# Optimization experiments

Measured on AMD Instinct MI355X. Metric: run time of the kernel, lower is better.

## Reference

```python
import jax, jax.numpy as jnp
import numpy as np

B, F, NQ, DT, TS, K = 16384, 256, 2048, 256, 16, 8
GH, SH, CALH = 128, 128, 16
SPD = DT + TS
SPH = max(int(SPD * 0.25), 16)
CD = DT + 3 + TS + 3  # h_base + y_base + 3 gate stats + z_top + |d_safe| + |d_spec| = 278
CH = max(int(CD * 0.25), 16)
RES_SCALE = 0.1


def _ln(x, g, b):
    m = x.mean(-1, keepdims=True)
    v = ((x - m) ** 2).mean(-1, keepdims=True)
    return (x - m) * jax.lax.rsqrt(v + 1e-5) * g + b


def _resmlp(x, lg, lb, w1, b1, w2, b2):
    h = jnp.maximum(_ln(x, lg, lb) @ w1 + b1, 0.0)
    return h @ w2 + b2


def setup_inputs() -> dict:
    key = jax.random.key(0)
    ks = iter(jax.random.split(key, 48))
    def nrm(shape, s=0.05):
        return jax.random.normal(next(ks), shape, jnp.float32) * s
    d = {}
    d["x_num"] = jax.random.normal(next(ks), (B, F), jnp.float32)
    d["robust_center"] = nrm((1, F), 0.1)
    d["robust_scale"] = jax.random.uniform(next(ks), (1, F), jnp.float32, 0.5, 1.5)
    d["quantile_sorted"] = jnp.sort(jax.random.normal(next(ks), (NQ, F), jnp.float32), axis=0)
    d["stem_w1"] = nrm((3, CALH)); d["stem_b1"] = jnp.zeros((CALH,))
    d["stem_w2"] = nrm((CALH, CALH)); d["stem_b2"] = jnp.zeros((CALH,))
    d["stem_w3"] = nrm((CALH, 1)); d["stem_b3"] = jnp.zeros((1,))
    d["gate_w1"] = nrm((F, GH)); d["gate_b1"] = jnp.zeros((GH,))
    d["gate_w2"] = nrm((GH, F)); d["gate_b2"] = jnp.zeros((F,))
    d["bb_w"] = nrm((F, DT)); d["bb_b"] = jnp.zeros((DT,))
    d["base_w"] = nrm((DT, 1)); d["base_b"] = jnp.zeros((1,))
    d["safe_lg"] = jnp.ones((DT,)); d["safe_lb"] = jnp.zeros((DT,))
    d["safe_w1"] = nrm((DT, SH)); d["safe_b1"] = jnp.zeros((SH,))
    d["safe_w2"] = nrm((SH, 1)); d["safe_b2"] = jnp.zeros((1,))
    d["top_w1"] = nrm((1, TS)); d["top_b1"] = jnp.zeros((TS,))
    d["top_w2"] = nrm((TS, TS)); d["top_b2"] = jnp.zeros((TS,))
    d["spec_lg"] = jnp.ones((SPD,)); d["spec_lb"] = jnp.zeros((SPD,))
    d["spec_w1"] = nrm((SPD, SPH)); d["spec_b1"] = jnp.zeros((SPH,))
    d["spec_w2"] = nrm((SPH, 1)); d["spec_b2"] = jnp.zeros((1,))
    d["conf_lg"] = jnp.ones((CD,)); d["conf_lb"] = jnp.zeros((CD,))
    d["conf_w1"] = nrm((CD, CH)); d["conf_b1"] = jnp.zeros((CH,))
    d["conf_w2"] = nrm((CH, 1)); d["conf_b2"] = jnp.full((1,), -2.0)  # gamma_init_bias
    return d


def _forward(x_num, robust_center, robust_scale, quantile_sorted,
             stem_w1, stem_b1, stem_w2, stem_b2, stem_w3, stem_b3,
             gate_w1, gate_b1, gate_w2, gate_b2,
             bb_w, bb_b, base_w, base_b,
             safe_lg, safe_lb, safe_w1, safe_b1, safe_w2, safe_b2,
             top_w1, top_b1, top_w2, top_b2,
             spec_lg, spec_lb, spec_w1, spec_b1, spec_w2, spec_b2,
             conf_lg, conf_lb, conf_w1, conf_b1, conf_w2, conf_b2):
    # --- calibration views ---
    x_robust = (x_num - robust_center) / robust_scale
    ranks = jax.vmap(jnp.searchsorted, in_axes=(1, 1), out_axes=1)(
        jax.lax.stop_gradient(quantile_sorted), jax.lax.stop_gradient(x_num))  # [B,F] int
    x_quant = jnp.clip(ranks.astype(jnp.float32) / (NQ - 1.0), 0.0, 1.0)
    x_views = jnp.stack([x_num, x_robust, x_quant], axis=-1)  # [B,F,3]
    h = jnp.maximum(x_views @ stem_w1 + stem_b1, 0.0)
    h = jnp.maximum(h @ stem_w2 + stem_b2, 0.0)
    resid = jnp.tanh((h @ stem_w3 + stem_b3)[..., 0])
    x_cal = x_num + RES_SCALE * resid
    # --- input gate ---
    g = jax.nn.sigmoid(jnp.maximum(x_cal @ gate_w1 + gate_b1, 0.0) @ gate_w2 + gate_b2)
    x_gated = x_cal * g
    # --- backbone (stand-in for TMLPBackbone.encode_hidden) ---
    h_base = jnp.maximum(x_gated @ bb_w + bb_b, 0.0)  # [B,DT]
    y_base = h_base @ base_w + base_b  # [B,1]
    gate_mean = g.mean(axis=1, keepdims=True)
    gate_max = g.max(axis=1, keepdims=True)
    gate_std = g.std(axis=1, keepdims=True)  # ddof=0, matches unbiased=False
    delta_safe = _resmlp(h_base, safe_lg, safe_lb, safe_w1, safe_b1, safe_w2, safe_b2)
    # --- top-k feature gather ---
    topk_g, topk_idx = jax.lax.top_k(g, K)
    topk_x = jnp.take_along_axis(x_cal, topk_idx, axis=1)
    topk_w = topk_g / (topk_g.sum(axis=1, keepdims=True) + 1e-6)
    xw = (topk_x * topk_w)[..., None]  # [B,K,1]
    tok = jnp.maximum(xw @ top_w1 + top_b1, 0.0) @ top_w2 + top_b2  # [B,K,TS]
    z_top = tok.mean(axis=1)  # [B,TS]
    delta_spec = _resmlp(jnp.concatenate([h_base, z_top], axis=1),
                         spec_lg, spec_lb, spec_w1, spec_b1, spec_w2, spec_b2)
    conf_in = jnp.concatenate([h_base, y_base, gate_mean, gate_max, gate_std,
                               z_top, jnp.abs(delta_safe), jnp.abs(delta_spec)], axis=1)
    gamma = jax.nn.sigmoid(_resmlp(conf_in, conf_lg, conf_lb, conf_w1, conf_b1, conf_w2, conf_b2))
    return (y_base + delta_safe + gamma * delta_spec)[:, 0]


def reference(x_num, robust_center, robust_scale, quantile_sorted,
              stem_w1, stem_b1, stem_w2, stem_b2, stem_w3, stem_b3,
              gate_w1, gate_b1, gate_w2, gate_b2,
              bb_w, bb_b, base_w, base_b,
              safe_lg, safe_lb, safe_w1, safe_b1, safe_w2, safe_b2,
              top_w1, top_b1, top_w2, top_b2,
              spec_lg, spec_lb, spec_w1, spec_b1, spec_w2, spec_b2,
              conf_lg, conf_lb, conf_w1, conf_b1, conf_w2, conf_b2):
    return _forward(x_num, robust_center, robust_scale, quantile_sorted,
                    stem_w1, stem_b1, stem_w2, stem_b2, stem_w3, stem_b3,
                    gate_w1, gate_b1, gate_w2, gate_b2,
                    bb_w, bb_b, base_w, base_b,
                    safe_lg, safe_lb, safe_w1, safe_b1, safe_w2, safe_b2,
                    top_w1, top_b1, top_w2, top_b2,
                    spec_lg, spec_lb, spec_w1, spec_b1, spec_w2, spec_b2,
                    conf_lg, conf_lb, conf_w1, conf_b1, conf_w2, conf_b2)
```

## Files before the change

kernel.cpp:

```cpp
#include <hip/hip_runtime.h>
#include <math.h>

static constexpr int B  = 16384;
static constexpr int F  = 256;
static constexpr int NQ = 2048;
static constexpr int TS = 16;
static constexpr int KTOP = 8;
static constexpr int SPD = 272;
static constexpr int SPH = 68;
static constexpr int CD  = 278;
static constexpr int CH  = 69;

typedef __attribute__((ext_vector_type(8))) short bf16x8;
typedef __attribute__((ext_vector_type(4))) float f32x4;

__device__ inline short f2bf(float f) {
    unsigned u = __builtin_bit_cast(unsigned, f);
    unsigned r = (u + 0x7FFF + ((u >> 16) & 1)) >> 16;
    return (short)r;
}
__device__ inline float bf2f(short s) {
    return __builtin_bit_cast(float, ((unsigned)(unsigned short)s) << 16);
}

__device__ inline float fast_tanh(float o) {
    o = fminf(fmaxf(o, -15.0f), 15.0f);
    float e = __expf(2.0f * o);
    return (e - 1.0f) / (e + 1.0f);
}

__device__ inline void prep_one(const float* W, short* T, int local,
                                int K, int N, int KP) {
    const int n = local / KP, k = local - n * KP;
    T[local] = (k < K && n < N) ? f2bf(W[k * N + n]) : (short)0;
}

__global__ __launch_bounds__(256) void k_prepall(
    const float* __restrict__ gate_w1, const float* __restrict__ gate_w2,
    const float* __restrict__ bb_w,    const float* __restrict__ safe_w1,
    const float* __restrict__ spec_w1, const float* __restrict__ conf_w1,
    const float* __restrict__ qs,
    short* __restrict__ w1t, short* __restrict__ w2t, short* __restrict__ bbt,
    short* __restrict__ sw1t, short* __restrict__ spw1t, short* __restrict__ cfw1t,
    float* __restrict__ qs_t)
{
    const int idx = blockIdx.x * 256 + threadIdx.x;
    if (idx < 32768)       prep_one(gate_w1, w1t,  idx,           256, 128, 256);
    else if (idx < 65536)  prep_one(gate_w2, w2t,  idx - 32768,   128, 256, 128);
    else if (idx < 131072) prep_one(bb_w,    bbt,  idx - 65536,   256, 256, 256);
    else if (idx < 163840) prep_one(safe_w1, sw1t, idx - 131072,  256, 128, 256);
    else if (idx < 200704) prep_one(spec_w1, spw1t, idx - 163840, 272, 68, 288);
    else if (idx < 237568) prep_one(conf_w1, cfw1t, idx - 200704, 278, 69, 288);
    else if (idx < 761856) {
        const int local = idx - 237568;
        const int f = local >> 11, q = local & 2047;
        qs_t[local] = qs[q * 256 + f];
    }
}

__global__ __launch_bounds__(256) void k_calib9(
    const float* __restrict__ x_num, const float* __restrict__ center,
    const float* __restrict__ scale, const float* __restrict__ qs,
    const float* __restrict__ qs_t,
    const float* __restrict__ sw1, const float* __restrict__ sb1,
    const float* __restrict__ sw2, const float* __restrict__ sb2,
    const float* __restrict__ sw3, const float* __restrict__ sb3,
    short* __restrict__ x_bf)
{
    __shared__ float cq[63 * 128];
    const int tid = threadIdx.x;
    const int fl = tid & 127;
    const int half = tid >> 7;
    const int fg = blockIdx.y;
    const int f = fg * 128 + fl;

    for (int idx = tid; idx < 63 * 128; idx += 256) {
        const int j = idx >> 7, f2 = idx & 127;
        cq[idx] = qs[(32 * (j + 1)) * 256 + fg * 128 + f2];
    }
    __syncthreads();

    const float c = center[f];
    const float inv_sc = 1.0f / scale[f];
    const float* colp = qs_t + (long)f * NQ;
    const long row_base = (long)blockIdx.x * 32 + half * 16;

#pragma unroll 1
    for (int grp = 0; grp < 2; ++grp) {
        const long r0 = row_base + grp * 8;
        float x[8], xr[8];
#pragma unroll
        for (int i = 0; i < 8; ++i) {
            x[i] = x_num[(r0 + i) * F + f];
            xr[i] = (x[i] - c) * inv_sc;
        }
        int lo[8], hi[8];
#pragma unroll
        for (int i = 0; i < 8; ++i) { lo[i] = 0; hi[i] = 63; }
#pragma unroll
        for (int it = 0; it < 6; ++it) {
            float qv[8]; int mid[8];
#pragma unroll
            for (int i = 0; i < 8; ++i) {
                mid[i] = (lo[i] + hi[i]) >> 1;
                qv[i] = cq[mid[i] * 128 + fl];
            }
#pragma unroll
            for (int i = 0; i < 8; ++i) {
                if (qv[i] < x[i]) lo[i] = mid[i] + 1; else hi[i] = mid[i];
            }
        }
        int base[8];
        {
            float pm[8];
#pragma unroll
            for (int i = 0; i < 8; ++i) pm[i] = colp[lo[i] * 32 + 16];
#pragma unroll
            for (int i = 0; i < 8; ++i)
                base[i] = lo[i] * 32 + ((pm[i] < x[i]) ? 16 : 0);
        }
        float xq[8];
#pragma unroll
        for (int i = 0; i < 8; ++i) {
            const float4* wp = reinterpret_cast<const float4*>(&colp[base[i]]);
            const float4 a = wp[0], b = wp[1], d = wp[2], e = wp[3];
            int cN = 0;
            cN += (a.x < x[i]); cN += (a.y < x[i]); cN += (a.z < x[i]); cN += (a.w < x[i]);
            cN += (b.x < x[i]); cN += (b.y < x[i]); cN += (b.z < x[i]); cN += (b.w < x[i]);
            cN += (d.x < x[i]); cN += (d.y < x[i]); cN += (d.z < x[i]); cN += (d.w < x[i]);
            cN += (e.x < x[i]); cN += (e.y < x[i]); cN += (e.z < x[i]); cN += (e.w < x[i]);
            const int rank = base[i] + cN;
            xq[i] = fminf((float)rank * (1.0f / (float)(NQ - 1)), 1.0f);
        }
#pragma unroll
        for (int hgrp = 0; hgrp < 2; ++hgrp) {
            const int o4 = hgrp * 4;
            float h2[4][16];
#pragma unroll
            for (int j = 0; j < 16; ++j) {
                const float bb = sb2[j];
#pragma unroll
                for (int i = 0; i < 4; ++i) h2[i][j] = bb;
            }
#pragma unroll 4
            for (int i16 = 0; i16 < 16; ++i16) {
                const float w0 = sw1[i16], w1v = sw1[16 + i16], w2v = sw1[32 + i16];
                const float bb = sb1[i16];
                float h1v[4];
#pragma unroll
                for (int i = 0; i < 4; ++i)
                    h1v[i] = fmaxf(bb + x[o4 + i] * w0 + xr[o4 + i] * w1v + xq[o4 + i] * w2v, 0.0f);
                float wv[16];
                const float4* wr = reinterpret_cast<const float4*>(&sw2[i16 * 16]);
                *reinterpret_cast<float4*>(&wv[0])  = wr[0];
                *reinterpret_cast<float4*>(&wv[4])  = wr[1];
                *reinterpret_cast<float4*>(&wv[8])  = wr[2];
                *reinterpret_cast<float4*>(&wv[12]) = wr[3];
#pragma unroll
                for (int j = 0; j < 16; ++j) {
#pragma unroll
                    for (int i = 0; i < 4; ++i) h2[i][j] += h1v[i] * wv[j];
                }
            }
            const float b3 = sb3[0];
            float o[4] = {b3, b3, b3, b3};
#pragma unroll
            for (int j = 0; j < 16; ++j) {
                const float w3v = sw3[j];
#pragma unroll
                for (int i = 0; i < 4; ++i) o[i] += fmaxf(h2[i][j], 0.0f) * w3v;
            }
#pragma unroll
            for (int i = 0; i < 4; ++i) {
                const float xc = x[o4 + i] + 0.1f * fast_tanh(o[i]);
                x_bf[(r0 + o4 + i) * F + f] = f2bf(xc);
            }
        }
    }
}

static constexpr int ST1 = 136;
static constexpr int ST2 = 264;

__global__ __launch_bounds__(256) void k_fused(
    const short* __restrict__ x_bf,
    const short* __restrict__ w1t, const float* __restrict__ gate_b1,
    const short* __restrict__ w2t, const float* __restrict__ gate_b2,
    const short* __restrict__ bbt, const float* __restrict__ bb_b,
    float* __restrict__ g, float* __restrict__ h_b)
{
    __shared__ short s_c1[32 * ST1];
    __shared__ short s_xg[32 * ST2];

    const int tid = threadIdx.x;
    const int wave = tid >> 6, lane = tid & 63;
    const int sub = lane & 15, quad = lane >> 4;
    const int wm = wave & 1, wn = wave >> 1;
    const long row0 = (long)blockIdx.x * 32;
    const long mrow = row0 + wm * 16 + sub;

    {
        f32x4 acc[4];
#pragma unroll
        for (int t = 0; t < 4; ++t) acc[t] = (f32x4){0, 0, 0, 0};
#pragma unroll
        for (int k0 = 0; k0 < 256; k0 += 32) {
            const bf16x8 af = *reinterpret_cast<const bf16x8*>(
                &x_bf[mrow * 256 + k0 + quad * 8]);
#pragma unroll
            for (int t = 0; t < 4; ++t) {
                const int col = wn * 64 + t * 16 + sub;
                const bf16x8 bf = *reinterpret_cast<const bf16x8*>(
                    &w1t[(long)col * 256 + k0 + quad * 8]);
                acc[t] = __builtin_amdgcn_mfma_f32_16x16x32_bf16(af, bf, acc[t], 0, 0, 0);
            }
        }
#pragma unroll
        for (int t = 0; t < 4; ++t) {
            const int col = wn * 64 + t * 16 + sub;
            const float bb = gate_b1[col];
#pragma unroll
            for (int r = 0; r < 4; ++r) {
                const int rowl = wm * 16 + quad * 4 + r;
                s_c1[rowl * ST1 + col] = f2bf(fmaxf(acc[t][r] + bb, 0.0f));
            }
        }
    }
    __syncthreads();

    {
        f32x4 acc[8];
#pragma unroll
        for (int t = 0; t < 8; ++t) acc[t] = (f32x4){0, 0, 0, 0};
#pragma unroll
        for (int k0 = 0; k0 < 128; k0 += 32) {
            const bf16x8 af = *reinterpret_cast<const bf16x8*>(
                &s_c1[(wm * 16 + sub) * ST1 + k0 + quad * 8]);
#pragma unroll
            for (int t = 0; t < 8; ++t) {
                const int col = wn * 128 + t * 16 + sub;
                const bf16x8 bf = *reinterpret_cast<const bf16x8*>(
                    &w2t[(long)col * 128 + k0 + quad * 8]);
                acc[t] = __builtin_amdgcn_mfma_f32_16x16x32_bf16(af, bf, acc[t], 0, 0, 0);
            }
        }
#pragma unroll
        for (int t = 0; t < 8; ++t) {
            const int col = wn * 128 + t * 16 + sub;
            const float bb = gate_b2[col];
#pragma unroll
            for (int r = 0; r < 4; ++r) {
                const int rowl = wm * 16 + quad * 4 + r;
                const float gv = 1.0f / (1.0f + __expf(-(acc[t][r] + bb)));
                g[(row0 + rowl) * 256 + col] = gv;
                const float xv = bf2f(x_bf[(row0 + rowl) * 256 + col]);
                s_xg[rowl * ST2 + col] = f2bf(xv * gv);
            }
        }
    }
    __syncthreads();

    {
        f32x4 acc[8];
#pragma unroll
        for (int t = 0; t < 8; ++t) acc[t] = (f32x4){0, 0, 0, 0};
#pragma unroll
        for (int k0 = 0; k0 < 256; k0 += 32) {
            const bf16x8 af = *reinterpret_cast<const bf16x8*>(
                &s_xg[(wm * 16 + sub) * ST2 + k0 + quad * 8]);
#pragma unroll
            for (int t = 0; t < 8; ++t) {
                const int col = wn * 128 + t * 16 + sub;
                const bf16x8 bf = *reinterpret_cast<const bf16x8*>(
                    &bbt[(long)col * 256 + k0 + quad * 8]);
                acc[t] = __builtin_amdgcn_mfma_f32_16x16x32_bf16(af, bf, acc[t], 0, 0, 0);
            }
        }
#pragma unroll
        for (int t = 0; t < 8; ++t) {
            const int col = wn * 128 + t * 16 + sub;
            const float bb = bb_b[col];
#pragma unroll
            for (int r = 0; r < 4; ++r) {
                const int rowl = wm * 16 + quad * 4 + r;
                h_b[(row0 + rowl) * 256 + col] = fmaxf(acc[t][r] + bb, 0.0f);
            }
        }
    }
}

__global__ __launch_bounds__(256) void k_topk2(
    const float* __restrict__ g, const short* __restrict__ x_bf,
    const float* __restrict__ tw1, const float* __restrict__ tb1,
    const float* __restrict__ tw2, const float* __restrict__ tb2,
    float* __restrict__ z_top, float* __restrict__ stats)
{
    const int wave = threadIdx.x >> 6, lane = threadIdx.x & 63;
    const long b = (long)blockIdx.x * 4 + wave;
    const long base = b * F;

    float gv[4];
#pragma unroll
    for (int i = 0; i < 4; ++i) gv[i] = g[base + lane + 64 * i];

    float s = gv[0] + gv[1] + gv[2] + gv[3];
    float mx = fmaxf(fmaxf(gv[0], gv[1]), fmaxf(gv[2], gv[3]));
    for (int m = 32; m; m >>= 1) {
        s  += __shfl_xor(s, m);
        mx  = fmaxf(mx, __shfl_xor(mx, m));
    }
    const float mean = s * (1.0f / 256.0f);
    float vs = 0.0f;
#pragma unroll
    for (int i = 0; i < 4; ++i) { float d = gv[i] - mean; vs += d * d; }
    for (int m = 32; m; m >>= 1) vs += __shfl_xor(vs, m);
    const float stdv = sqrtf(vs * (1.0f / 256.0f));

    float cur[4]; int curi[4];
#pragma unroll
    for (int i = 0; i < 4; ++i) { cur[i] = gv[i]; curi[i] = lane + 64 * i; }
    float tv[KTOP]; int ti[KTOP]; float vsum = 0.0f;
    for (int r = 0; r < KTOP; ++r) {
        float bv = cur[0]; int bi = curi[0];
#pragma unroll
        for (int i = 1; i < 4; ++i)
            if (cur[i] > bv || (cur[i] == bv && curi[i] < bi)) { bv = cur[i]; bi = curi[i]; }
        for (int m = 32; m; m >>= 1) {
            float ov = __shfl_xor(bv, m);
            int   oi = __shfl_xor(bi, m);
            if (ov > bv || (ov == bv && oi < bi)) { bv = ov; bi = oi; }
        }
        tv[r] = bv; ti[r] = bi; vsum += bv;
#pragma unroll
        for (int i = 0; i < 4; ++i) if (curi[i] == bi) cur[i] = -INFINITY;
    }
    const float denom = 1.0f / (vsum + 1e-6f);

    float hm = 0.0f;
    if (lane < 16) {
        for (int k = 0; k < KTOP; ++k) {
            const float xk = bf2f(x_bf[base + ti[k]]);
            const float xw = xk * (tv[k] * denom);
            hm += fmaxf(xw * tw1[lane] + tb1[lane], 0.0f);
        }
        hm *= (1.0f / (float)KTOP);
    }
    float z = (lane < 16) ? tb2[lane] : 0.0f;
#pragma unroll
    for (int j = 0; j < 16; ++j) {
        const float hj = __shfl(hm, j);
        if (lane < 16) z += hj * tw2[j * 16 + lane];
    }
    if (lane < 16) z_top[b * TS + lane] = z;
    if (lane == 0) {
        stats[b * 4 + 0] = mean;
        stats[b * 4 + 1] = mx;
        stats[b * 4 + 2] = stdv;
    }
}

static constexpr int HST = 260;
static constexpr int AST = 312;

template<int KP>
__device__ __forceinline__ void head_mfma16(
    const short* sa, const short* __restrict__ Wt,
    const float* __restrict__ b1v, const float* __restrict__ w2v, int Nreal,
    float (*s_red)[16], int wave, int sub, int quad)
{
    f32x4 acc[2];
#pragma unroll
    for (int t = 0; t < 2; ++t) acc[t] = (f32x4){0, 0, 0, 0};
#pragma unroll
    for (int k0 = 0; k0 < KP; k0 += 32) {
        const bf16x8 af = *reinterpret_cast<const bf16x8*>(
            &sa[sub * AST + k0 + quad * 8]);
#pragma unroll
        for (int t = 0; t < 2; ++t) {
            const int col = wave * 32 + t * 16 + sub;
            const bf16x8 bf = *reinterpret_cast<const bf16x8*>(
                &Wt[(long)col * KP + k0 + quad * 8]);
            acc[t] = __builtin_amdgcn_mfma_f32_16x16x32_bf16(af, bf, acc[t], 0, 0, 0);
        }
    }
    float rsum[4] = {0, 0, 0, 0};
#pragma unroll
    for (int t = 0; t < 2; ++t) {
        const int col = wave * 32 + t * 16 + sub;
        const float bb = (col < Nreal) ? b1v[col] : 0.0f;
        const float ww = (col < Nreal) ? w2v[col] : 0.0f;
#pragma unroll
        for (int rr = 0; rr < 4; ++rr)
            rsum[rr] += fmaxf(acc[t][rr] + bb, 0.0f) * ww;
    }
#pragma unroll
    for (int rr = 0; rr < 4; ++rr)
        for (int m = 1; m < 16; m <<= 1) rsum[rr] += __shfl_xor(rsum[rr], m);
    if (sub == 0) {
#pragma unroll
        for (int rr = 0; rr < 4; ++rr)
            s_red[wave][quad * 4 + rr] = rsum[rr];
    }
}

__global__ __launch_bounds__(256) void k_tail3(
    const float* __restrict__ h_base, const float* __restrict__ z_top,
    const float* __restrict__ gstats,
    const float* __restrict__ base_w, const float* __restrict__ base_b,
    const float* __restrict__ safe_lg, const float* __restrict__ safe_lb,
    const short* __restrict__ sw1t, const float* __restrict__ safe_b1,
    const float* __restrict__ safe_w2, const float* __restrict__ safe_b2,
    const float* __restrict__ spec_lg, const float* __restrict__ spec_lb,
    const short* __restrict__ spw1t, const float* __restrict__ spec_b1,
    const float* __restrict__ spec_w2, const float* __restrict__ spec_b2,
    const float* __restrict__ conf_lg, const float* __restrict__ conf_lb,
    const short* __restrict__ cfw1t, const float* __restrict__ conf_b1,
    const float* __restrict__ conf_w2, const float* __restrict__ conf_b2,
    float* __restrict__ out)
{
    __shared__ float s_h[16 * HST];
    __shared__ short s_a[16 * AST];
    __shared__ float s_z[16 * 16];
    __shared__ float s_g[16 * 4];
    __shared__ float s_sc[16 * 14];
    __shared__ float s_red[4][16];

    const int tid = threadIdx.x;
    const int wave = tid >> 6, lane = tid & 63;
    const int sub = lane & 15, quad = lane >> 4;
    const long row0 = (long)blockIdx.x * 16;

    for (int idx = tid; idx < 16 * 64; idx += 256) {
        const int r = idx >> 6, q = idx & 63;
        *reinterpret_cast<float4*>(&s_h[r * HST + q * 4]) =
            *reinterpret_cast<const float4*>(&h_base[(row0 + r) * 256 + q * 4]);
    }
    if (tid < 256) s_z[tid] = z_top[row0 * 16 + tid];
    if (tid < 64) s_g[tid] = gstats[row0 * 4 + tid];
    __syncthreads();

    {
        const int r = tid >> 4, l16 = tid & 15;
        float S = 0.0f, SS = 0.0f, Y = 0.0f;
#pragma unroll
        for (int i = 0; i < 16; ++i) {
            const int k = l16 + 16 * i;
            const float v = s_h[r * HST + k];
            S += v; SS += v * v; Y += v * base_w[k];
        }
        const float z0 = s_z[r * 16 + l16];
        float Sz = z0, SSz = z0 * z0;
#pragma unroll
        for (int m = 1; m < 16; m <<= 1) {
            S += __shfl_xor(S, m); SS += __shfl_xor(SS, m); Y += __shfl_xor(Y, m);
            Sz += __shfl_xor(Sz, m); SSz += __shfl_xor(SSz, m);
        }
        if (l16 == 0) {
            float* sc = &s_sc[r * 14];
            sc[0] = S; sc[1] = SS; sc[2] = Sz; sc[3] = SSz;
            sc[4] = Y + base_b[0];
            const float mu = S * (1.0f / 256.0f);
            sc[5] = mu;
            sc[6] = rsqrtf(SS * (1.0f / 256.0f) - mu * mu + 1e-5f);
            const float musp = (S + Sz) * (1.0f / (float)SPD);
            sc[7] = musp;
            sc[8] = rsqrtf((SS + SSz) * (1.0f / (float)SPD) - musp * musp + 1e-5f);
        }
    }
    __syncthreads();

    for (int idx = tid; idx < 16 * 128; idx += 256) {
        const int r = idx >> 7, k = (idx & 127) * 2;
        const float mu = s_sc[r * 14 + 5], rs = s_sc[r * 14 + 6];
        const float v0 = (s_h[r * HST + k] - mu) * rs * safe_lg[k] + safe_lb[k];
        const float v1 = (s_h[r * HST + k + 1] - mu) * rs * safe_lg[k + 1] + safe_lb[k + 1];
        const unsigned pk = (unsigned)(unsigned short)f2bf(v0) |
                            ((unsigned)(unsigned short)f2bf(v1) << 16);
        *reinterpret_cast<unsigned*>(&s_a[r * AST + k]) = pk;
    }
    __syncthreads();

    head_mfma16<256>(s_a, sw1t, safe_b1, safe_w2, 128, s_red, wave, sub, quad);
    __syncthreads();

    if (tid < 16)
        s_sc[tid * 14 + 9] = s_red[0][tid] + s_red[1][tid] + s_red[2][tid] + s_red[3][tid] + safe_b2[0];
    for (int idx = tid; idx < 16 * 144; idx += 256) {
        const int r = idx / 144, k = (idx - r * 144) * 2;
        const float mu = s_sc[r * 14 + 7], rs = s_sc[r * 14 + 8];
        float vv[2];
#pragma unroll
        for (int h = 0; h < 2; ++h) {
            const int kk = k + h;
            float raw = (kk < 256) ? s_h[r * HST + kk]
                       : (kk < SPD) ? s_z[r * 16 + kk - 256] : 0.0f;
            vv[h] = (kk < SPD) ? (raw - mu) * rs * spec_lg[kk] + spec_lb[kk] : 0.0f;
        }
        const unsigned pk = (unsigned)(unsigned short)f2bf(vv[0]) |
                            ((unsigned)(unsigned short)f2bf(vv[1]) << 16);
        *reinterpret_cast<unsigned*>(&s_a[r * AST + k]) = pk;
    }
    __syncthreads();

    head_mfma16<288>(s_a, spw1t, spec_b1, spec_w2, SPH, s_red, wave, sub, quad);
    __syncthreads();

    if (tid < 16) {
        float* sc = &s_sc[tid * 14];
        const float dsp = s_red[0][tid] + s_red[1][tid] + s_red[2][tid] + s_red[3][tid] + spec_b2[0];
        sc[10] = dsp;
        const float yb = sc[4];
        const float gm = s_g[tid * 4 + 0], gx = s_g[tid * 4 + 1], gs = s_g[tid * 4 + 2];
        const float ads = fabsf(sc[9]), adp = fabsf(dsp);
        const float es = yb + gm + gx + gs + ads + adp;
        const float eq = yb * yb + gm * gm + gx * gx + gs * gs + ads * ads + adp * adp;
        const float muc = (sc[0] + sc[2] + es) * (1.0f / (float)CD);
        sc[11] = muc;
        sc[12] = rsqrtf((sc[1] + sc[3] + eq) * (1.0f / (float)CD) - muc * muc + 1e-5f);
    }
    __syncthreads();

    for (int idx = tid; idx < 16 * 144; idx += 256) {
        const int r = idx / 144, k = (idx - r * 144) * 2;
        const float mu = s_sc[r * 14 + 11], rs = s_sc[r * 14 + 12];
        float vv[2];
#pragma unroll
        for (int h = 0; h < 2; ++h) {
            const int kk = k + h;
            float raw;
            if (kk < 256)       raw = s_h[r * HST + kk];
            else if (kk == 256) raw = s_sc[r * 14 + 4];
            else if (kk == 257) raw = s_g[r * 4 + 0];
            else if (kk == 258) raw = s_g[r * 4 + 1];
            else if (kk == 259) raw = s_g[r * 4 + 2];
            else if (kk < 276)  raw = s_z[r * 16 + kk - 260];
            else if (kk == 276) raw = fabsf(s_sc[r * 14 + 9]);
            else if (kk == 277) raw = fabsf(s_sc[r * 14 + 10]);
            else                raw = 0.0f;
            vv[h] = (kk < CD) ? (raw - mu) * rs * conf_lg[kk] + conf_lb[kk] : 0.0f;
        }
        const unsigned pk = (unsigned)(unsigned short)f2bf(vv[0]) |
                            ((unsigned)(unsigned short)f2bf(vv[1]) << 16);
        *reinterpret_cast<unsigned*>(&s_a[r * AST + k]) = pk;
    }
    __syncthreads();

    head_mfma16<288>(s_a, cfw1t, conf_b1, conf_w2, CH, s_red, wave, sub, quad);
    __syncthreads();

    if (tid < 16) {
        const float* sc = &s_sc[tid * 14];
        const float gamma = 1.0f / (1.0f + __expf(
            -(s_red[0][tid] + s_red[1][tid] + s_red[2][tid] + s_red[3][tid] + conf_b2[0])));
        out[row0 + tid] = sc[4] + sc[9] + gamma * sc[10];
    }
}

extern "C" void kernel_launch(void* const* d_in, const int* in_sizes, int n_in,
                              void* d_out, int out_size, void* d_ws, size_t ws_size,
                              hipStream_t stream)
{
    const float* x_num   = (const float*)d_in[0];
    const float* center  = (const float*)d_in[1];
    const float* scale   = (const float*)d_in[2];
    const float* qs      = (const float*)d_in[3];
    const float* stem_w1 = (const float*)d_in[4];
    const float* stem_b1 = (const float*)d_in[5];
    const float* stem_w2 = (const float*)d_in[6];
    const float* stem_b2 = (const float*)d_in[7];
    const float* stem_w3 = (const float*)d_in[8];
    const float* stem_b3 = (const float*)d_in[9];
    const float* gate_w1 = (const float*)d_in[10];
    const float* gate_b1 = (const float*)d_in[11];
    const float* gate_w2 = (const float*)d_in[12];
    const float* gate_b2 = (const float*)d_in[13];
    const float* bb_w    = (const float*)d_in[14];
    const float* bb_b    = (const float*)d_in[15];
    const float* base_w  = (const float*)d_in[16];
    const float* base_b  = (const float*)d_in[17];
    const float* safe_lg = (const float*)d_in[18];
    const float* safe_lb = (const float*)d_in[19];
    const float* safe_w1 = (const float*)d_in[20];
    const float* safe_b1 = (const float*)d_in[21];
    const float* safe_w2 = (const float*)d_in[22];
    const float* safe_b2 = (const float*)d_in[23];
    const float* top_w1  = (const float*)d_in[24];
    const float* top_b1  = (const float*)d_in[25];
    const float* top_w2  = (const float*)d_in[26];
    const float* top_b2  = (const float*)d_in[27];
    const float* spec_lg = (const float*)d_in[28];
    const float* spec_lb = (const float*)d_in[29];
    const float* spec_w1 = (const float*)d_in[30];
    const float* spec_b1 = (const float*)d_in[31];
    const float* spec_w2 = (const float*)d_in[32];
    const float* spec_b2 = (const float*)d_in[33];
    const float* conf_lg = (const float*)d_in[34];
    const float* conf_lb = (const float*)d_in[35];
    const float* conf_w1 = (const float*)d_in[36];
    const float* conf_b1 = (const float*)d_in[37];
    const float* conf_w2 = (const float*)d_in[38];
    const float* conf_b2 = (const float*)d_in[39];

    float* ws    = (float*)d_ws;
    float* x_cal = ws;
    float* g_h   = x_cal + (long)B * 256;
    float* g     = g_h   + (long)B * 128;
    float* h_b   = g     + (long)B * 256;
    float* z_top = h_b   + (long)B * 256;
    float* gstat = z_top + (long)B * 16;
    short* w1t   = (short*)(gstat + (long)B * 4);
    short* w2t   = w1t   + 128 * 256;
    short* bbt   = w2t   + 256 * 128;
    short* sw1t  = bbt   + 256 * 256;
    short* spw1t = sw1t  + 128 * 256;
    short* cfw1t = spw1t + 128 * 288;
    float* qs_t  = h_b;
    short* x_bf  = (short*)g_h;
    float* out   = (float*)d_out;

    k_prepall<<<2976, 256, 0, stream>>>(gate_w1, gate_w2, bb_w, safe_w1, spec_w1,
                                        conf_w1, qs,
                                        w1t, w2t, bbt, sw1t, spw1t, cfw1t, qs_t);
    k_calib9<<<dim3(512, 2), 256, 0, stream>>>(x_num, center, scale, qs, qs_t,
                                               stem_w1, stem_b1, stem_w2, stem_b2,
                                               stem_w3, stem_b3, x_bf);
    k_fused<<<512, 256, 0, stream>>>(x_bf, w1t, gate_b1, w2t, gate_b2, bbt, bb_b,
                                     g, h_b);
    k_topk2<<<B / 4, 256, 0, stream>>>(g, x_bf, top_w1, top_b1, top_w2, top_b2,
                                       z_top, gstat);
    k_tail3<<<B / 16, 256, 0, stream>>>(h_b, z_top, gstat,
                                        base_w, base_b,
                                        safe_lg, safe_lb, sw1t, safe_b1, safe_w2, safe_b2,
                                        spec_lg, spec_lb, spw1t, spec_b1, spec_w2, spec_b2,
                                        conf_lg, conf_lb, cfw1t, conf_b1, conf_w2, conf_b2,
                                        out);
}
```

Before: 314.1 us.

## Fuse gate MLP, top-k, backbone and heads into one kernel

Merges the gate/backbone GEMM kernel, the per-row top-k kernel and the tail heads kernel into one kernel processing 16 rows per block. The gate values and backbone activations stay in shared memory (backbone stored as bf16) instead of round-tripping g and h_b through global memory. Row statistics are reduced directly from the MFMA epilogue. This removes two launches and large intermediate global traffic, but halves the rows per block for the GEMMs, so weight reuse per block drops. It also adds bf16 rounding of h_base before the layer norms.

```diff
diff --git a/kernel.cpp b/kernel.cpp
--- a/kernel.cpp
+++ b/kernel.cpp
@@ -179,188 +179,11 @@
     }
 }
 
-static constexpr int ST1 = 136;
-static constexpr int ST2 = 264;
-
-__global__ __launch_bounds__(256) void k_fused(
-    const short* __restrict__ x_bf,
-    const short* __restrict__ w1t, const float* __restrict__ gate_b1,
-    const short* __restrict__ w2t, const float* __restrict__ gate_b2,
-    const short* __restrict__ bbt, const float* __restrict__ bb_b,
-    float* __restrict__ g, float* __restrict__ h_b)
-{
-    __shared__ short s_c1[32 * ST1];
-    __shared__ short s_xg[32 * ST2];
-
-    const int tid = threadIdx.x;
-    const int wave = tid >> 6, lane = tid & 63;
-    const int sub = lane & 15, quad = lane >> 4;
-    const int wm = wave & 1, wn = wave >> 1;
-    const long row0 = (long)blockIdx.x * 32;
-    const long mrow = row0 + wm * 16 + sub;
-
-    {
-        f32x4 acc[4];
-#pragma unroll
-        for (int t = 0; t < 4; ++t) acc[t] = (f32x4){0, 0, 0, 0};
-#pragma unroll
-        for (int k0 = 0; k0 < 256; k0 += 32) {
-            const bf16x8 af = *reinterpret_cast<const bf16x8*>(
-                &x_bf[mrow * 256 + k0 + quad * 8]);
-#pragma unroll
-            for (int t = 0; t < 4; ++t) {
-                const int col = wn * 64 + t * 16 + sub;
-                const bf16x8 bf = *reinterpret_cast<const bf16x8*>(
-                    &w1t[(long)col * 256 + k0 + quad * 8]);
-                acc[t] = __builtin_amdgcn_mfma_f32_16x16x32_bf16(af, bf, acc[t], 0, 0, 0);
-            }
-        }
-#pragma unroll
-        for (int t = 0; t < 4; ++t) {
-            const int col = wn * 64 + t * 16 + sub;
-            const float bb = gate_b1[col];
-#pragma unroll
-            for (int r = 0; r < 4; ++r) {
-                const int rowl = wm * 16 + quad * 4 + r;
-                s_c1[rowl * ST1 + col] = f2bf(fmaxf(acc[t][r] + bb, 0.0f));
-            }
-        }
-    }
-    __syncthreads();
-
-    {
-        f32x4 acc[8];
-#pragma unroll
-        for (int t = 0; t < 8; ++t) acc[t] = (f32x4){0, 0, 0, 0};
-#pragma unroll
-        for (int k0 = 0; k0 < 128; k0 += 32) {
-            const bf16x8 af = *reinterpret_cast<const bf16x8*>(
-                &s_c1[(wm * 16 + sub) * ST1 + k0 + quad * 8]);
-#pragma unroll
-            for (int t = 0; t < 8; ++t) {
-                const int col = wn * 128 + t * 16 + sub;
-                const bf16x8 bf = *reinterpret_cast<const bf16x8*>(
-                    &w2t[(long)col * 128 + k0 + quad * 8]);
-                acc[t] = __builtin_amdgcn_mfma_f32_16x16x32_bf16(af, bf, acc[t], 0, 0, 0);
-            }
-        }
-#pragma unroll
-        for (int t = 0; t < 8; ++t) {
-            const int col = wn * 128 + t * 16 + sub;
-            const float bb = gate_b2[col];
-#pragma unroll
-            for (int r = 0; r < 4; ++r) {
-                const int rowl = wm * 16 + quad * 4 + r;
-                const float gv = 1.0f / (1.0f + __expf(-(acc[t][r] + bb)));
-                g[(row0 + rowl) * 256 + col] = gv;
-                const float xv = bf2f(x_bf[(row0 + rowl) * 256 + col]);
-                s_xg[rowl * ST2 + col] = f2bf(xv * gv);
-            }
-        }
-    }
-    __syncthreads();
-
-    {
-        f32x4 acc[8];
-#pragma unroll
-        for (int t = 0; t < 8; ++t) acc[t] = (f32x4){0, 0, 0, 0};
-#pragma unroll
-        for (int k0 = 0; k0 < 256; k0 += 32) {
-            const bf16x8 af = *reinterpret_cast<const bf16x8*>(
-                &s_xg[(wm * 16 + sub) * ST2 + k0 + quad * 8]);
-#pragma unroll
-            for (int t = 0; t < 8; ++t) {
-                const int col = wn * 128 + t * 16 + sub;
-                const bf16x8 bf = *reinterpret_cast<const bf16x8*>(
-                    &bbt[(long)col * 256 + k0 + quad * 8]);
-                acc[t] = __builtin_amdgcn_mfma_f32_16x16x32_bf16(af, bf, acc[t], 0, 0, 0);
-            }
-        }
-#pragma unroll
-        for (int t = 0; t < 8; ++t) {
-            const int col = wn * 128 + t * 16 + sub;
-            const float bb = bb_b[col];
-#pragma unroll
-            for (int r = 0; r < 4; ++r) {
-                const int rowl = wm * 16 + quad * 4 + r;
-                h_b[(row0 + rowl) * 256 + col] = fmaxf(acc[t][r] + bb, 0.0f);
-            }
-        }
-    }
-}
-
-__global__ __launch_bounds__(256) void k_topk2(
-    const float* __restrict__ g, const short* __restrict__ x_bf,
-    const float* __restrict__ tw1, const float* __restrict__ tb1,
-    const float* __restrict__ tw2, const float* __restrict__ tb2,
-    float* __restrict__ z_top, float* __restrict__ stats)
-{
-    const int wave = threadIdx.x >> 6, lane = threadIdx.x & 63;
-    const long b = (long)blockIdx.x * 4 + wave;
-    const long base = b * F;
-
-    float gv[4];
-#pragma unroll
-    for (int i = 0; i < 4; ++i) gv[i] = g[base + lane + 64 * i];
-
-    float s = gv[0] + gv[1] + gv[2] + gv[3];
-    float mx = fmaxf(fmaxf(gv[0], gv[1]), fmaxf(gv[2], gv[3]));
-    for (int m = 32; m; m >>= 1) {
-        s  += __shfl_xor(s, m);
-        mx  = fmaxf(mx, __shfl_xor(mx, m));
-    }
-    const float mean = s * (1.0f / 256.0f);
-    float vs = 0.0f;
-#pragma unroll
-    for (int i = 0; i < 4; ++i) { float d = gv[i] - mean; vs += d * d; }
-    for (int m = 32; m; m >>= 1) vs += __shfl_xor(vs, m);
-    const float stdv = sqrtf(vs * (1.0f / 256.0f));
-
-    float cur[4]; int curi[4];
-#pragma unroll
-    for (int i = 0; i < 4; ++i) { cur[i] = gv[i]; curi[i] = lane + 64 * i; }
-    float tv[KTOP]; int ti[KTOP]; float vsum = 0.0f;
-    for (int r = 0; r < KTOP; ++r) {
-        float bv = cur[0]; int bi = curi[0];
-#pragma unroll
-        for (int i = 1; i < 4; ++i)
-            if (cur[i] > bv || (cur[i] == bv && curi[i] < bi)) { bv = cur[i]; bi = curi[i]; }
-        for (int m = 32; m; m >>= 1) {
-            float ov = __shfl_xor(bv, m);
-            int   oi = __shfl_xor(bi, m);
-            if (ov > bv || (ov == bv && oi < bi)) { bv = ov; bi = oi; }
-        }
-        tv[r] = bv; ti[r] = bi; vsum += bv;
-#pragma unroll
-        for (int i = 0; i < 4; ++i) if (curi[i] == bi) cur[i] = -INFINITY;
-    }
-    const float denom = 1.0f / (vsum + 1e-6f);
-
-    float hm = 0.0f;
-    if (lane < 16) {
-        for (int k = 0; k < KTOP; ++k) {
-            const float xk = bf2f(x_bf[base + ti[k]]);
-            const float xw = xk * (tv[k] * denom);
-            hm += fmaxf(xw * tw1[lane] + tb1[lane], 0.0f);
-        }
-        hm *= (1.0f / (float)KTOP);
-    }
-    float z = (lane < 16) ? tb2[lane] : 0.0f;
-#pragma unroll
-    for (int j = 0; j < 16; ++j) {
-        const float hj = __shfl(hm, j);
-        if (lane < 16) z += hj * tw2[j * 16 + lane];
-    }
-    if (lane < 16) z_top[b * TS + lane] = z;
-    if (lane == 0) {
-        stats[b * 4 + 0] = mean;
-        stats[b * 4 + 1] = mx;
-        stats[b * 4 + 2] = stdv;
-    }
-}
-
-static constexpr int HST = 260;
-static constexpr int AST = 312;
+static constexpr int MR   = 16;
+static constexpr int GST  = 260;
+static constexpr int AST  = 312;
+static constexpr int HBST = 264;
+static constexpr int C1ST = 136;
 
 template<int KP>
 __device__ __forceinline__ void head_mfma16(
@@ -403,10 +226,14 @@
     }
 }
 
-__global__ __launch_bounds__(256) void k_tail3(
-    const float* __restrict__ h_base, const float* __restrict__ z_top,
-    const float* __restrict__ gstats,
+__global__ __launch_bounds__(256) void k_mega(
+    const short* __restrict__ x_bf,
+    const short* __restrict__ w1t, const float* __restrict__ gate_b1,
+    const short* __restrict__ w2t, const float* __restrict__ gate_b2,
+    const short* __restrict__ bbt, const float* __restrict__ bb_b,
     const float* __restrict__ base_w, const float* __restrict__ base_b,
+    const float* __restrict__ tw1, const float* __restrict__ tb1,
+    const float* __restrict__ tw2, const float* __restrict__ tb2,
     const float* __restrict__ safe_lg, const float* __restrict__ safe_lb,
     const short* __restrict__ sw1t, const float* __restrict__ safe_b1,
     const float* __restrict__ safe_w2, const float* __restrict__ safe_b2,
@@ -418,99 +245,269 @@
     const float* __restrict__ conf_w2, const float* __restrict__ conf_b2,
     float* __restrict__ out)
 {
-    __shared__ float s_h[16 * HST];
-    __shared__ short s_a[16 * AST];
-    __shared__ float s_z[16 * 16];
-    __shared__ float s_g[16 * 4];
-    __shared__ float s_sc[16 * 14];
-    __shared__ float s_red[4][16];
+    __shared__ float s_g[MR * GST];
+    __shared__ short s_u1[MR * AST];
+    __shared__ short s_c1[MR * C1ST];
+    __shared__ short s_hbb[MR * HBST];
+    __shared__ float s_z[MR * 16];
+    __shared__ float s_sc[MR * 16];
+    __shared__ float s_redS[4][16], s_redSS[4][16], s_redY[4][16];
 
     const int tid = threadIdx.x;
     const int wave = tid >> 6, lane = tid & 63;
     const int sub = lane & 15, quad = lane >> 4;
-    const long row0 = (long)blockIdx.x * 16;
-
-    for (int idx = tid; idx < 16 * 64; idx += 256) {
-        const int r = idx >> 6, q = idx & 63;
-        *reinterpret_cast<float4*>(&s_h[r * HST + q * 4]) =
-            *reinterpret_cast<const float4*>(&h_base[(row0 + r) * 256 + q * 4]);
-    }
-    if (tid < 256) s_z[tid] = z_top[row0 * 16 + tid];
-    if (tid < 64) s_g[tid] = gstats[row0 * 4 + tid];
-    __syncthreads();
+    const long row0 = (long)blockIdx.x * MR;
 
     {
-        const int r = tid >> 4, l16 = tid & 15;
-        float S = 0.0f, SS = 0.0f, Y = 0.0f;
-#pragma unroll
-        for (int i = 0; i < 16; ++i) {
-            const int k = l16 + 16 * i;
-            const float v = s_h[r * HST + k];
-            S += v; SS += v * v; Y += v * base_w[k];
-        }
-        const float z0 = s_z[r * 16 + l16];
-        float Sz = z0, SSz = z0 * z0;
+        f32x4 acc[2];
+#pragma unroll
+        for (int t = 0; t < 2; ++t) acc[t] = (f32x4){0, 0, 0, 0};
+#pragma unroll
+        for (int k0 = 0; k0 < 256; k0 += 32) {
+            const bf16x8 af = *reinterpret_cast<const bf16x8*>(
+                &x_bf[(row0 + sub) * 256 + k0 + quad * 8]);
+#pragma unroll
+            for (int t = 0; t < 2; ++t) {
+                const int col = wave * 32 + t * 16 + sub;
+                const bf16x8 bf = *reinterpret_cast<const bf16x8*>(
+                    &w1t[(long)col * 256 + k0 + quad * 8]);
+                acc[t] = __builtin_amdgcn_mfma_f32_16x16x32_bf16(af, bf, acc[t], 0, 0, 0);
+            }
+        }
+#pragma unroll
+        for (int t = 0; t < 2; ++t) {
+            const int col = wave * 32 + t * 16 + sub;
+            const float bb = gate_b1[col];
+#pragma unroll
+            for (int r = 0; r < 4; ++r)
+                s_c1[(quad * 4 + r) * C1ST + col] = f2bf(fmaxf(acc[t][r] + bb, 0.0f));
+        }
+    }
+    __syncthreads();
+
+    {
+        f32x4 acc[4];
+#pragma unroll
+        for (int t = 0; t < 4; ++t) acc[t] = (f32x4){0, 0, 0, 0};
+#pragma unroll
+        for (int k0 = 0; k0 < 128; k0 += 32) {
+            const bf16x8 af = *reinterpret_cast<const bf16x8*>(
+                &s_c1[sub * C1ST + k0 + quad * 8]);
+#pragma unroll
+            for (int t = 0; t < 4; ++t) {
+                const int col = wave * 64 + t * 16 + sub;
+                const bf16x8 bf = *reinterpret_cast<const bf16x8*>(
+                    &w2t[(long)col * 128 + k0 + quad * 8]);
+                acc[t] = __builtin_amdgcn_mfma_f32_16x16x32_bf16(af, bf, acc[t], 0, 0, 0);
+            }
+        }
+#pragma unroll
+        for (int t = 0; t < 4; ++t) {
+            const int col = wave * 64 + t * 16 + sub;
+            const float bb = gate_b2[col];
+#pragma unroll
+            for (int r = 0; r < 4; ++r)
+                s_g[(quad * 4 + r) * GST + col] =
+                    1.0f / (1.0f + __expf(-(acc[t][r] + bb)));
+        }
+    }
+    __syncthreads();
+
+#pragma unroll 1
+    for (int rr = 0; rr < 4; ++rr) {
+        const int row = wave * 4 + rr;
+        float gv[4];
+#pragma unroll
+        for (int i = 0; i < 4; ++i) gv[i] = s_g[row * GST + lane + 64 * i];
+
+        float s = gv[0] + gv[1] + gv[2] + gv[3];
+        float mx = fmaxf(fmaxf(gv[0], gv[1]), fmaxf(gv[2], gv[3]));
+        for (int m = 32; m; m >>= 1) {
+            s  += __shfl_xor(s, m);
+            mx  = fmaxf(mx, __shfl_xor(mx, m));
+        }
+        const float mean = s * (1.0f / 256.0f);
+        float vs = 0.0f;
+#pragma unroll
+        for (int i = 0; i < 4; ++i) { float d = gv[i] - mean; vs += d * d; }
+        for (int m = 32; m; m >>= 1) vs += __shfl_xor(vs, m);
+        const float stdv = sqrtf(vs * (1.0f / 256.0f));
+
+        float cur[4]; int curi[4];
+#pragma unroll
+        for (int i = 0; i < 4; ++i) { cur[i] = gv[i]; curi[i] = lane + 64 * i; }
+        float tv[KTOP]; int ti[KTOP]; float vsum = 0.0f;
+        for (int r = 0; r < KTOP; ++r) {
+            float bv = cur[0]; int bi = curi[0];
+#pragma unroll
+            for (int i = 1; i < 4; ++i)
+                if (cur[i] > bv || (cur[i] == bv && curi[i] < bi)) { bv = cur[i]; bi = curi[i]; }
+            for (int m = 32; m; m >>= 1) {
+                float ov = __shfl_xor(bv, m);
+                int   oi = __shfl_xor(bi, m);
+                if (ov > bv || (ov == bv && oi < bi)) { bv = ov; bi = oi; }
+            }
+            tv[r] = bv; ti[r] = bi; vsum += bv;
+#pragma unroll
+            for (int i = 0; i < 4; ++i) if (curi[i] == bi) cur[i] = -INFINITY;
+        }
+        const float denom = 1.0f / (vsum + 1e-6f);
+
+        float hm = 0.0f;
+        if (lane < 16) {
+            for (int k = 0; k < KTOP; ++k) {
+                const float xk = bf2f(x_bf[(row0 + row) * 256 + ti[k]]);
+                const float xw = xk * (tv[k] * denom);
+                hm += fmaxf(xw * tw1[lane] + tb1[lane], 0.0f);
+            }
+            hm *= (1.0f / (float)KTOP);
+        }
+        float z = (lane < 16) ? tb2[lane] : 0.0f;
+#pragma unroll
+        for (int j = 0; j < 16; ++j) {
+            const float hj = __shfl(hm, j);
+            if (lane < 16) z += hj * tw2[j * 16 + lane];
+        }
+        if (lane < 16) s_z[row * 16 + lane] = z;
+        float zz = (lane < 16) ? z : 0.0f;
+        float zz2 = zz * zz;
 #pragma unroll
         for (int m = 1; m < 16; m <<= 1) {
-            S += __shfl_xor(S, m); SS += __shfl_xor(SS, m); Y += __shfl_xor(Y, m);
-            Sz += __shfl_xor(Sz, m); SSz += __shfl_xor(SSz, m);
-        }
-        if (l16 == 0) {
-            float* sc = &s_sc[r * 14];
-            sc[0] = S; sc[1] = SS; sc[2] = Sz; sc[3] = SSz;
-            sc[4] = Y + base_b[0];
-            const float mu = S * (1.0f / 256.0f);
-            sc[5] = mu;
-            sc[6] = rsqrtf(SS * (1.0f / 256.0f) - mu * mu + 1e-5f);
-            const float musp = (S + Sz) * (1.0f / (float)SPD);
-            sc[7] = musp;
-            sc[8] = rsqrtf((SS + SSz) * (1.0f / (float)SPD) - musp * musp + 1e-5f);
-        }
-    }
-    __syncthreads();
-
-    for (int idx = tid; idx < 16 * 128; idx += 256) {
+            zz += __shfl_xor(zz, m); zz2 += __shfl_xor(zz2, m);
+        }
+        if (lane == 0) {
+            float* sc = &s_sc[row * 16];
+            sc[2] = zz; sc[3] = zz2;
+            sc[13] = mean; sc[14] = mx; sc[15] = stdv;
+        }
+    }
+    __syncthreads();
+
+    for (int idx = tid; idx < MR * 128; idx += 256) {
         const int r = idx >> 7, k = (idx & 127) * 2;
-        const float mu = s_sc[r * 14 + 5], rs = s_sc[r * 14 + 6];
-        const float v0 = (s_h[r * HST + k] - mu) * rs * safe_lg[k] + safe_lb[k];
-        const float v1 = (s_h[r * HST + k + 1] - mu) * rs * safe_lg[k + 1] + safe_lb[k + 1];
+        const unsigned xp = *reinterpret_cast<const unsigned*>(
+            &x_bf[(row0 + r) * 256 + k]);
+        const float x0 = bf2f((short)(xp & 0xFFFF));
+        const float x1 = bf2f((short)(xp >> 16));
+        const float v0 = x0 * s_g[r * GST + k];
+        const float v1 = x1 * s_g[r * GST + k + 1];
         const unsigned pk = (unsigned)(unsigned short)f2bf(v0) |
                             ((unsigned)(unsigned short)f2bf(v1) << 16);
-        *reinterpret_cast<unsigned*>(&s_a[r * AST + k]) = pk;
-    }
-    __syncthreads();
-
-    head_mfma16<256>(s_a, sw1t, safe_b1, safe_w2, 128, s_red, wave, sub, quad);
-    __syncthreads();
-
-    if (tid < 16)
-        s_sc[tid * 14 + 9] = s_red[0][tid] + s_red[1][tid] + s_red[2][tid] + s_red[3][tid] + safe_b2[0];
-    for (int idx = tid; idx < 16 * 144; idx += 256) {
+        *reinterpret_cast<unsigned*>(&s_u1[r * AST + k]) = pk;
+    }
+    __syncthreads();
+
+    {
+        f32x4 acc[4];
+#pragma unroll
+        for (int t = 0; t < 4; ++t) acc[t] = (f32x4){0, 0, 0, 0};
+#pragma unroll
+        for (int k0 = 0; k0 < 256; k0 += 32) {
+            const bf16x8 af = *reinterpret_cast<const bf16x8*>(
+                &s_u1[sub * AST + k0 + quad * 8]);
+#pragma unroll
+            for (int t = 0; t < 4; ++t) {
+                const int col = wave * 64 + t * 16 + sub;
+                const bf16x8 bf = *reinterpret_cast<const bf16x8*>(
+                    &bbt[(long)col * 256 + k0 + quad * 8]);
+                acc[t] = __builtin_amdgcn_mfma_f32_16x16x32_bf16(af, bf, acc[t], 0, 0, 0);
+            }
+        }
+        float Sp[4] = {0,0,0,0}, SSp[4] = {0,0,0,0}, Yp[4] = {0,0,0,0};
+#pragma unroll
+        for (int t = 0; t < 4; ++t) {
+            const int col = wave * 64 + t * 16 + sub;
+            const float bb = bb_b[col];
+            const float bw = base_w[col];
+#pragma unroll
+            for (int r = 0; r < 4; ++r) {
+                const float h = fmaxf(acc[t][r] + bb, 0.0f);
+                s_hbb[(quad * 4 + r) * HBST + col] = f2bf(h);
+                Sp[r] += h; SSp[r] += h * h; Yp[r] += h * bw;
+            }
+        }
+#pragma unroll
+        for (int r = 0; r < 4; ++r) {
+#pragma unroll
+            for (int m = 1; m < 16; m <<= 1) {
+                Sp[r] += __shfl_xor(Sp[r], m);
+                SSp[r] += __shfl_xor(SSp[r], m);
+                Yp[r] += __shfl_xor(Yp[r], m);
+            }
+        }
+        if (sub == 0) {
+#pragma unroll
+            for (int r = 0; r < 4; ++r) {
+                s_redS[wave][quad * 4 + r] = Sp[r];
+                s_redSS[wave][quad * 4 + r] = SSp[r];
+                s_redY[wave][quad * 4 + r] = Yp[r];
+            }
+        }
+    }
+    __syncthreads();
+
+    if (tid < MR) {
+        float S = 0, SS = 0, Y = 0;
+#pragma unroll
+        for (int w = 0; w < 4; ++w) {
+            S += s_redS[w][tid]; SS += s_redSS[w][tid]; Y += s_redY[w][tid];
+        }
+        float* sc = &s_sc[tid * 16];
+        sc[0] = S; sc[1] = SS;
+        sc[4] = Y + base_b[0];
+        const float mu = S * (1.0f / 256.0f);
+        sc[5] = mu;
+        sc[6] = rsqrtf(SS * (1.0f / 256.0f) - mu * mu + 1e-5f);
+        const float musp = (S + sc[2]) * (1.0f / (float)SPD);
+        sc[7] = musp;
+        sc[8] = rsqrtf((SS + sc[3]) * (1.0f / (float)SPD) - musp * musp + 1e-5f);
+    }
+    __syncthreads();
+
+    for (int idx = tid; idx < MR * 128; idx += 256) {
+        const int r = idx >> 7, k = (idx & 127) * 2;
+        const float mu = s_sc[r * 16 + 5], rs = s_sc[r * 16 + 6];
+        const float h0 = bf2f(s_hbb[r * HBST + k]);
+        const float h1 = bf2f(s_hbb[r * HBST + k + 1]);
+        const float v0 = (h0 - mu) * rs * safe_lg[k] + safe_lb[k];
+        const float v1 = (h1 - mu) * rs * safe_lg[k + 1] + safe_lb[k + 1];
+        const unsigned pk = (unsigned)(unsigned short)f2bf(v0) |
+                            ((unsigned)(unsigned short)f2bf(v1) << 16);
+        *reinterpret_cast<unsigned*>(&s_u1[r * AST + k]) = pk;
+    }
+    __syncthreads();
+    head_mfma16<256>(s_u1, sw1t, safe_b1, safe_w2, 128, s_redS, wave, sub, quad);
+    __syncthreads();
+
+    if (tid < MR)
+        s_sc[tid * 16 + 9] = s_redS[0][tid] + s_redS[1][tid] + s_redS[2][tid] +
+                             s_redS[3][tid] + safe_b2[0];
+    for (int idx = tid; idx < MR * 144; idx += 256) {
         const int r = idx / 144, k = (idx - r * 144) * 2;
-        const float mu = s_sc[r * 14 + 7], rs = s_sc[r * 14 + 8];
+        const float mu = s_sc[r * 16 + 7], rs = s_sc[r * 16 + 8];
         float vv[2];
 #pragma unroll
         for (int h = 0; h < 2; ++h) {
             const int kk = k + h;
-            float raw = (kk < 256) ? s_h[r * HST + kk]
+            float raw = (kk < 256) ? bf2f(s_hbb[r * HBST + kk])
                        : (kk < SPD) ? s_z[r * 16 + kk - 256] : 0.0f;
             vv[h] = (kk < SPD) ? (raw - mu) * rs * spec_lg[kk] + spec_lb[kk] : 0.0f;
         }
         const unsigned pk = (unsigned)(unsigned short)f2bf(vv[0]) |
                             ((unsigned)(unsigned short)f2bf(vv[1]) << 16);
-        *reinterpret_cast<unsigned*>(&s_a[r * AST + k]) = pk;
-    }
-    __syncthreads();
-
-    head_mfma16<288>(s_a, spw1t, spec_b1, spec_w2, SPH, s_red, wave, sub, quad);
-    __syncthreads();
-
-    if (tid < 16) {
-        float* sc = &s_sc[tid * 14];
-        const float dsp = s_red[0][tid] + s_red[1][tid] + s_red[2][tid] + s_red[3][tid] + spec_b2[0];
+        *reinterpret_cast<unsigned*>(&s_u1[r * AST + k]) = pk;
+    }
+    __syncthreads();
+    head_mfma16<288>(s_u1, spw1t, spec_b1, spec_w2, SPH, s_redS, wave, sub, quad);
+    __syncthreads();
+
+    if (tid < MR) {
+        float* sc = &s_sc[tid * 16];
+        const float dsp = s_redS[0][tid] + s_redS[1][tid] + s_redS[2][tid] +
+                          s_redS[3][tid] + spec_b2[0];
         sc[10] = dsp;
         const float yb = sc[4];
-        const float gm = s_g[tid * 4 + 0], gx = s_g[tid * 4 + 1], gs = s_g[tid * 4 + 2];
+        const float gm = sc[13], gx = sc[14], gs = sc[15];
         const float ads = fabsf(sc[9]), adp = fabsf(dsp);
         const float es = yb + gm + gx + gs + ads + adp;
         const float eq = yb * yb + gm * gm + gx * gx + gs * gs + ads * ads + adp * adp;
@@ -520,38 +517,37 @@
     }
     __syncthreads();
 
-    for (int idx = tid; idx < 16 * 144; idx += 256) {
+    for (int idx = tid; idx < MR * 144; idx += 256) {
         const int r = idx / 144, k = (idx - r * 144) * 2;
-        const float mu = s_sc[r * 14 + 11], rs = s_sc[r * 14 + 12];
+        const float mu = s_sc[r * 16 + 11], rs = s_sc[r * 16 + 12];
         float vv[2];
 #pragma unroll
         for (int h = 0; h < 2; ++h) {
             const int kk = k + h;
             float raw;
-            if (kk < 256)       raw = s_h[r * HST + kk];
-            else if (kk == 256) raw = s_sc[r * 14 + 4];
-            else if (kk == 257) raw = s_g[r * 4 + 0];
-            else if (kk == 258) raw = s_g[r * 4 + 1];
-            else if (kk == 259) raw = s_g[r * 4 + 2];
+            if (kk < 256)       raw = bf2f(s_hbb[r * HBST + kk]);
+            else if (kk == 256) raw = s_sc[r * 16 + 4];
+            else if (kk == 257) raw = s_sc[r * 16 + 13];
+            else if (kk == 258) raw = s_sc[r * 16 + 14];
+            else if (kk == 259) raw = s_sc[r * 16 + 15];
             else if (kk < 276)  raw = s_z[r * 16 + kk - 260];
-            else if (kk == 276) raw = fabsf(s_sc[r * 14 + 9]);
-            else if (kk == 277) raw = fabsf(s_sc[r * 14 + 10]);
+            else if (kk == 276) raw = fabsf(s_sc[r * 16 + 9]);
+            else if (kk == 277) raw = fabsf(s_sc[r * 16 + 10]);
             else                raw = 0.0f;
             vv[h] = (kk < CD) ? (raw - mu) * rs * conf_lg[kk] + conf_lb[kk] : 0.0f;
         }
         const unsigned pk = (unsigned)(unsigned short)f2bf(vv[0]) |
                             ((unsigned)(unsigned short)f2bf(vv[1]) << 16);
-        *reinterpret_cast<unsigned*>(&s_a[r * AST + k]) = pk;
-    }
-    __syncthreads();
-
-    head_mfma16<288>(s_a, cfw1t, conf_b1, conf_w2, CH, s_red, wave, sub, quad);
-    __syncthreads();
-
-    if (tid < 16) {
-        const float* sc = &s_sc[tid * 14];
+        *reinterpret_cast<unsigned*>(&s_u1[r * AST + k]) = pk;
+    }
+    __syncthreads();
+    head_mfma16<288>(s_u1, cfw1t, conf_b1, conf_w2, CH, s_redS, wave, sub, quad);
+    __syncthreads();
+
+    if (tid < MR) {
+        const float* sc = &s_sc[tid * 16];
         const float gamma = 1.0f / (1.0f + __expf(
-            -(s_red[0][tid] + s_red[1][tid] + s_red[2][tid] + s_red[3][tid] + conf_b2[0])));
+            -(s_redS[0][tid] + s_redS[1][tid] + s_redS[2][tid] + s_redS[3][tid] + conf_b2[0])));
         out[row0 + tid] = sc[4] + sc[9] + gamma * sc[10];
     }
 }
@@ -624,14 +620,12 @@
     k_calib9<<<dim3(512, 2), 256, 0, stream>>>(x_num, center, scale, qs, qs_t,
                                                stem_w1, stem_b1, stem_w2, stem_b2,
                                                stem_w3, stem_b3, x_bf);
-    k_fused<<<512, 256, 0, stream>>>(x_bf, w1t, gate_b1, w2t, gate_b2, bbt, bb_b,
-                                     g, h_b);
-    k_topk2<<<B / 4, 256, 0, stream>>>(g, x_bf, top_w1, top_b1, top_w2, top_b2,
-                                       z_top, gstat);
-    k_tail3<<<B / 16, 256, 0, stream>>>(h_b, z_top, gstat,
-                                        base_w, base_b,
-                                        safe_lg, safe_lb, sw1t, safe_b1, safe_w2, safe_b2,
-                                        spec_lg, spec_lb, spw1t, spec_b1, spec_w2, spec_b2,
-                                        conf_lg, conf_lb, cfw1t, conf_b1, conf_w2, conf_b2,
-                                        out);
-}
+    k_mega<<<B / MR, 256, 0, stream>>>(x_bf,
+                                       w1t, gate_b1, w2t, gate_b2, bbt, bb_b,
+                                       base_w, base_b,
+                                       top_w1, top_b1, top_w2, top_b2,
+                                       safe_lg, safe_lb, sw1t, safe_b1, safe_w2, safe_b2,
+                                       spec_lg, spec_lb, spw1t, spec_b1, spec_w2, spec_b2,
+                                       conf_lg, conf_lb, cfw1t, conf_b1, conf_w2, conf_b2,
+                                       out);
+}
```

Result: slower. 333.0 us (+6.0%).
